# Kernel tuning notes

Measured on AMD Instinct MI355X. Metric: run time of the kernel, lower is better.

The kernel has to match this reference:

```python
import jax, jax.numpy as jnp
import numpy as np
from jax import lax

T, B, INP, HS, OUT = 256, 128, 1024, 1024, 1024


def setup_inputs() -> dict:
    key = jax.random.key(0)
    ks = jax.random.split(key, 7)
    s = 1.0 / np.sqrt(HS)  # scale params to keep tanh out of deep saturation
    return {
        "data": jax.random.normal(ks[0], (T, B, INP), jnp.float32),
        "W_ih": jax.random.normal(ks[1], (INP, HS), jnp.float32) * s,
        "W_hh": jax.random.normal(ks[2], (HS, HS), jnp.float32) * s,
        "b_i": jax.random.normal(ks[3], (HS,), jnp.float32) * s,
        "b_h": jax.random.normal(ks[4], (HS,), jnp.float32) * s,
        "W_out": jax.random.normal(ks[5], (OUT, HS), jnp.float32) * s,
        "b_out": jax.random.normal(ks[6], (OUT,), jnp.float32) * s,
    }


def reference(data, W_ih, W_hh, b_i, b_h, W_out, b_out):
    # Elman RNN: h_{t+1} = tanh(x_t @ W_ih + b_i + h_t @ W_hh + b_h)
    bias = b_i + b_h
    h0 = jnp.zeros((data.shape[1], W_hh.shape[0]), data.dtype)

    def step(h, x_t):
        h_new = jnp.tanh(x_t @ W_ih + h @ W_hh + bias)
        return h_new, None

    h_final, _ = lax.scan(step, h0, data)
    # nn.Linear: out = h @ W_out.T + b_out
    return h_final @ W_out.T + b_out
```

## Files before the change

### kernel.cpp

```cpp
#include <hip/hip_runtime.h>
#include <hip/hip_bf16.h>
#include <math.h>


typedef __attribute__((ext_vector_type(8))) short bf16x8;
typedef __attribute__((ext_vector_type(4))) float f32x4;
typedef __attribute__((ext_vector_type(4))) unsigned int u32x4;
typedef __attribute__((ext_vector_type(2))) unsigned int u32x2;

#define TT 256
#define BB 128
#define HS 1024
#define H_ELEMS (BB * HS)
#define POISON32 0xAAAAAAAAu

__device__ __forceinline__ short f2bf(float x) {
  __hip_bfloat16 b = __float2bfloat16(x);
  return *reinterpret_cast<short*>(&b);
}
__device__ __forceinline__ float bf2f(unsigned short s) {
  unsigned int u = ((unsigned int)s) << 16;
  float f;
  __builtin_memcpy(&f, &u, 4);
  return f;
}
__device__ __forceinline__ float fast_exp2(float x) {
#if __has_builtin(__builtin_amdgcn_exp2f)
  return __builtin_amdgcn_exp2f(x);
#else
  return exp2f(x);
#endif
}
__device__ __forceinline__ float fast_rcp(float x) {
#if __has_builtin(__builtin_amdgcn_rcpf)
  return __builtin_amdgcn_rcpf(x);
#else
  return 1.0f / x;
#endif
}
__device__ __forceinline__ float fast_tanh(float x) {
  float xc = fminf(fmaxf(x, -9.0f), 9.0f);
  float e = fast_exp2(2.8853900817779268f * xc);
  return (e - 1.0f) * fast_rcp(e + 1.0f);
}

__device__ __forceinline__ void mall_load_b128(u32x4* dst, const void* p) {
  asm volatile("global_load_dwordx4 %0, %1, off sc0 sc1" : "=v"(*dst) : "v"(p) : "memory");
}
__device__ __forceinline__ void mall_store_b64(void* p, u32x2 v) {
  asm volatile("global_store_dwordx2 %0, %1, off sc0 sc1" :: "v"(p), "v"(v) : "memory");
}
__device__ __forceinline__ void mall_store_b32(void* p, unsigned v) {
  asm volatile("global_store_dword %0, %1, off sc0 sc1" :: "v"(p), "v"(v) : "memory");
}
__device__ __forceinline__ unsigned mall_poll_b32(const void* p) {
  unsigned v;
  asm volatile("global_load_dword %0, %1, off sc0 sc1" : "=v"(v) : "v"(p) : "memory");
  asm volatile("s_waitcnt vmcnt(0)" : "+v"(v));
  return v;
}
__device__ __forceinline__ void wait_vm0() {
  asm volatile("s_waitcnt vmcnt(0)" ::: "memory");
}
#define TIE4(d)                                                         \
  asm volatile("s_waitcnt vmcnt(0)"                                     \
               : "+v"(d[0]), "+v"(d[1]), "+v"(d[2]), "+v"(d[3]))

__global__ __launch_bounds__(256) void cvt_data(const float* __restrict__ src,
                                                __hip_bfloat16* __restrict__ dst) {
  size_t i = ((size_t)blockIdx.x * 256 + threadIdx.x) * 8;
  f32x4 a = *reinterpret_cast<const f32x4*>(src + i);
  f32x4 b = *reinterpret_cast<const f32x4*>(src + i + 4);
  bf16x8 v;
  v[0] = f2bf(a[0]); v[1] = f2bf(a[1]); v[2] = f2bf(a[2]); v[3] = f2bf(a[3]);
  v[4] = f2bf(b[0]); v[5] = f2bf(b[1]); v[6] = f2bf(b[2]); v[7] = f2bf(b[3]);
  *reinterpret_cast<bf16x8*>(dst + i) = v;
}

__global__ __launch_bounds__(256) void cvt_tr(const float* __restrict__ src,
                                              __hip_bfloat16* __restrict__ dst) {
  __shared__ __hip_bfloat16 T[64][72];
  const int tid = threadIdx.x;
  const int k0 = blockIdx.y * 64, n0 = blockIdx.x * 64;
  const int r = tid >> 4, c4 = (tid & 15) * 4;
#pragma unroll
  for (int p = 0; p < 4; ++p) {
    int kk = r + p * 16;
    f32x4 v = *reinterpret_cast<const f32x4*>(src + (size_t)(k0 + kk) * 1024 + n0 + c4);
#pragma unroll
    for (int j = 0; j < 4; ++j) T[c4 + j][kk] = __float2bfloat16(v[j]);
  }
  __syncthreads();
  const int rr = tid >> 3, u = tid & 7;
#pragma unroll
  for (int p = 0; p < 2; ++p) {
    int R = rr + p * 32;
    *reinterpret_cast<bf16x8*>(dst + (size_t)(n0 + R) * 1024 + k0 + u * 8) =
        *reinterpret_cast<const bf16x8*>(&T[R][u * 8]);
  }
}

template <bool ABF>
__global__ __launch_bounds__(256) void gemm_xw2(
    const void* __restrict__ Ain,
    const __hip_bfloat16* __restrict__ Bt,
    const float* __restrict__ b_i,
    const float* __restrict__ b_h,
    __hip_bfloat16* __restrict__ P) {
  __shared__ __hip_bfloat16 As[128][72];
  __shared__ __hip_bfloat16 Bs[128][72];

  const int tid = threadIdx.x;
  const int m0 = blockIdx.y * 128, n0 = blockIdx.x * 128;
  const int wave = tid >> 6, lane = tid & 63;
  const int wm = wave & 1, wn = wave >> 1;
  const int quad = lane >> 4, l16 = lane & 15;
  const int sr = tid >> 3, su = tid & 7;

  f32x4 acc[4][4] = {};

  for (int k0 = 0; k0 < 1024; k0 += 64) {
    __syncthreads();
#pragma unroll
    for (int p = 0; p < 4; ++p) {
      int row = sr + p * 32;
      bf16x8 av;
      if (ABF) {
        av = *reinterpret_cast<const bf16x8*>(
            (const __hip_bfloat16*)Ain + (size_t)(m0 + row) * 1024 + k0 + su * 8);
      } else {
        const float* ap = (const float*)Ain + (size_t)(m0 + row) * 1024 + k0 + su * 8;
        f32x4 x = *reinterpret_cast<const f32x4*>(ap);
        f32x4 y = *reinterpret_cast<const f32x4*>(ap + 4);
        av[0] = f2bf(x[0]); av[1] = f2bf(x[1]); av[2] = f2bf(x[2]); av[3] = f2bf(x[3]);
        av[4] = f2bf(y[0]); av[5] = f2bf(y[1]); av[6] = f2bf(y[2]); av[7] = f2bf(y[3]);
      }
      *reinterpret_cast<bf16x8*>(&As[row][su * 8]) = av;
      bf16x8 bv = *reinterpret_cast<const bf16x8*>(
          Bt + (size_t)(n0 + row) * 1024 + k0 + su * 8);
      *reinterpret_cast<bf16x8*>(&Bs[row][su * 8]) = bv;
    }
    __syncthreads();
#pragma unroll
    for (int kk = 0; kk < 2; ++kk) {
      bf16x8 af[4], bfr[4];
#pragma unroll
      for (int mi = 0; mi < 4; ++mi)
        af[mi] = *reinterpret_cast<const bf16x8*>(&As[wm * 64 + mi * 16 + l16][kk * 32 + quad * 8]);
#pragma unroll
      for (int ni = 0; ni < 4; ++ni)
        bfr[ni] = *reinterpret_cast<const bf16x8*>(&Bs[wn * 64 + ni * 16 + l16][kk * 32 + quad * 8]);
#pragma unroll
      for (int mi = 0; mi < 4; ++mi)
#pragma unroll
        for (int ni = 0; ni < 4; ++ni)
          acc[mi][ni] = __builtin_amdgcn_mfma_f32_16x16x32_bf16(af[mi], bfr[ni], acc[mi][ni], 0, 0, 0);
    }
  }

  float bias[4];
#pragma unroll
  for (int ni = 0; ni < 4; ++ni) {
    int col = n0 + wn * 64 + ni * 16 + l16;
    bias[ni] = b_i[col] + b_h[col];
  }
#pragma unroll
  for (int mi = 0; mi < 4; ++mi)
#pragma unroll
    for (int ni = 0; ni < 4; ++ni) {
      int row = m0 + wm * 64 + mi * 16 + quad * 4;
      int col = n0 + wn * 64 + ni * 16 + l16;
#pragma unroll
      for (int r = 0; r < 4; ++r)
        P[(size_t)(row + r) * 1024 + col] = __float2bfloat16(acc[mi][ni][r] + bias[ni]);
    }
}

__global__ __launch_bounds__(512, 2) void rnn_scan8(
    const __hip_bfloat16* __restrict__ P,
    const float* __restrict__ W_hh,
    __hip_bfloat16* __restrict__ hslots) {
  __shared__ __hip_bfloat16 Wt[32 * 1024];
  __shared__ __hip_bfloat16 Ht[16 * 1024];
  __shared__ __hip_bfloat16 Cs[16 * 132];

  const int tid = threadIdx.x;
  const int m = blockIdx.x & 7;
  const int ng = blockIdx.x >> 3;
  const int m0 = m * 16, n0 = ng * 128;

  const int wv = tid >> 6, lane = tid & 63;
  const int quad = lane >> 4, l16 = lane & 15;
  const int colloc = wv * 16 + l16;
  const int col = n0 + colloc;
  const int nl = (wv & 1) * 16 + l16;
  const int xorl = l16 & 7;
  const int r16 = tid >> 5;
  const int s32 = tid & 31;

  bf16x8 wreg[32];
  for (int cch = 0; cch < 4; ++cch) {
    if (cch) __syncthreads();
    const int nb = n0 + cch * 32;
    for (int i = tid; i < 32 * 1024 / 4; i += 512) {
      int nq = i & 7, k = i >> 3;
      f32x4 v = *reinterpret_cast<const f32x4*>(W_hh + (size_t)k * 1024 + nb + nq * 4);
#pragma unroll
      for (int j = 0; j < 4; ++j) {
        int nll = nq * 4 + j;
        int sg = (k >> 3) ^ (nll & 7);
        Wt[nll * 1024 + sg * 8 + (k & 7)] = __float2bfloat16(v[j]);
      }
    }
    __syncthreads();
    if ((wv >> 1) == cch) {
#pragma unroll
      for (int wi = 0; wi < 32; ++wi) {
        int G = wi * 4 + quad;
        int sg = G ^ (nl & 7);
        wreg[wi] = *reinterpret_cast<const bf16x8*>(&Wt[nl * 1024 + sg * 8]);
      }
    }
  }
  __syncthreads();

  for (int t = 0; t < TT; ++t) {
    const __hip_bfloat16* hc = hslots + (size_t)t * H_ELEMS;
    __hip_bfloat16* hn = hslots + (size_t)(t + 1) * H_ELEMS;

    const __hip_bfloat16* Pt =
        P + (size_t)t * H_ELEMS + (size_t)(m0 + quad * 4) * 1024 + col;
    unsigned short pv[4];
#pragma unroll
    for (int r = 0; r < 4; ++r)
      pv[r] = *reinterpret_cast<const unsigned short*>(Pt + (size_t)r * 1024);

    const char* src = (const char*)(hc + (size_t)(m0 + r16) * 1024) + s32 * 16;
    u32x4 d[4];
    {
      int g = 0;
      for (;;) {
        mall_load_b128(&d[0], src);
        mall_load_b128(&d[1], src + 512);
        mall_load_b128(&d[2], src + 1024);
        mall_load_b128(&d[3], src + 1536);
        TIE4(d);
        bool ok = true;
#pragma unroll
        for (int i = 0; i < 4; ++i)
#pragma unroll
          for (int w2 = 0; w2 < 4; ++w2)
            ok &= (d[i][w2] != POISON32);
        if (ok || ++g >= (1 << 14)) break;
      }
    }
#pragma unroll
    for (int i = 0; i < 4; ++i) {
      int u = s32 + i * 32;
      int gp = u ^ (r16 & 7) ^ (u >> 4);
      *reinterpret_cast<u32x4*>(&Ht[r16 * 1024 + gp * 8]) = d[i];
    }
    __syncthreads();

    f32x4 acc[4] = {{0.f, 0.f, 0.f, 0.f}, {0.f, 0.f, 0.f, 0.f},
                    {0.f, 0.f, 0.f, 0.f}, {0.f, 0.f, 0.f, 0.f}};
#pragma unroll
    for (int c = 0; c < 8; ++c) {
#pragma unroll
      for (int j = 0; j < 4; ++j) {
        int G = c * 16 + j * 4 + quad;
        int gp = G ^ xorl ^ c;
        bf16x8 af = *reinterpret_cast<const bf16x8*>(&Ht[l16 * 1024 + gp * 8]);
        acc[j] = __builtin_amdgcn_mfma_f32_16x16x32_bf16(af, wreg[c * 4 + j], acc[j], 0, 0, 0);
      }
    }

#pragma unroll
    for (int r = 0; r < 4; ++r) {
      float s = (acc[0][r] + acc[1][r]) + (acc[2][r] + acc[3][r]) + bf2f(pv[r]);
      Cs[(quad * 4 + r) * 132 + colloc] = __float2bfloat16(fast_tanh(s));
    }
    __syncthreads();
    {
      u32x2 val = *reinterpret_cast<const u32x2*>(&Cs[r16 * 132 + s32 * 4]);
      mall_store_b64(hn + (size_t)(m0 + r16) * 1024 + n0 + s32 * 4, val);
    }
  }
  wait_vm0();
}

__global__ __launch_bounds__(512, 2) void rnn_scan7(
    const __hip_bfloat16* __restrict__ P,
    const float* __restrict__ W_hh,
    __hip_bfloat16* __restrict__ hbuf,
    unsigned* __restrict__ flags) {
  __shared__ __hip_bfloat16 Wt[32 * 1024];
  __shared__ __hip_bfloat16 Ht[16 * 1024];
  __shared__ __hip_bfloat16 Cs[16 * 132];

  const int tid = threadIdx.x;
  const int m = blockIdx.x & 7;
  const int ng = blockIdx.x >> 3;
  const int m0 = m * 16, n0 = ng * 128;

  const int wv = tid >> 6, lane = tid & 63;
  const int quad = lane >> 4, l16 = lane & 15;
  const int colloc = wv * 16 + l16;
  const int col = n0 + colloc;
  const int nl = (wv & 1) * 16 + l16;
  const int xorl = l16 & 7;
  const int r16 = tid >> 5;
  const int s32 = tid & 31;
  unsigned* gflags = flags + m * 8;

  bf16x8 wreg[32];
  for (int cch = 0; cch < 4; ++cch) {
    if (cch) __syncthreads();
    const int nb = n0 + cch * 32;
    for (int i = tid; i < 32 * 1024 / 4; i += 512) {
      int nq = i & 7, k = i >> 3;
      f32x4 v = *reinterpret_cast<const f32x4*>(W_hh + (size_t)k * 1024 + nb + nq * 4);
#pragma unroll
      for (int j = 0; j < 4; ++j) {
        int nll = nq * 4 + j;
        int sg = (k >> 3) ^ (nll & 7);
        Wt[nll * 1024 + sg * 8 + (k & 7)] = __float2bfloat16(v[j]);
      }
    }
    __syncthreads();
    if ((wv >> 1) == cch) {
#pragma unroll
      for (int wi = 0; wi < 32; ++wi) {
        int G = wi * 4 + quad;
        int sg = G ^ (nl & 7);
        wreg[wi] = *reinterpret_cast<const bf16x8*>(&Wt[nl * 1024 + sg * 8]);
      }
    }
  }
  __syncthreads();

  for (int t = 0; t < TT; ++t) {
    const __hip_bfloat16* hc = hbuf + (size_t)(t & 1) * H_ELEMS;
    __hip_bfloat16* hn = hbuf + (size_t)((t + 1) & 1) * H_ELEMS;

    const __hip_bfloat16* Pt =
        P + (size_t)t * H_ELEMS + (size_t)(m0 + quad * 4) * 1024 + col;
    unsigned short pv[4];
#pragma unroll
    for (int r = 0; r < 4; ++r)
      pv[r] = *reinterpret_cast<const unsigned short*>(Pt + (size_t)r * 1024);

    if (t > 0) {
      if (tid < 8) {
        const unsigned* fp = gflags + tid;
        int g = 0;
        while (mall_poll_b32(fp) < (unsigned)t && ++g < (1 << 18)) {}
      }
      __syncthreads();
    }

    {
      const char* src = (const char*)(hc + (size_t)(m0 + r16) * 1024) + s32 * 16;
      u32x4 d[4];
      mall_load_b128(&d[0], src);
      mall_load_b128(&d[1], src + 512);
      mall_load_b128(&d[2], src + 1024);
      mall_load_b128(&d[3], src + 1536);
      TIE4(d);
#pragma unroll
      for (int i = 0; i < 4; ++i) {
        int u = s32 + i * 32;
        int gp = u ^ (r16 & 7) ^ (u >> 4);
        *reinterpret_cast<u32x4*>(&Ht[r16 * 1024 + gp * 8]) = d[i];
      }
    }
    __syncthreads();

    f32x4 acc[4] = {{0.f, 0.f, 0.f, 0.f}, {0.f, 0.f, 0.f, 0.f},
                    {0.f, 0.f, 0.f, 0.f}, {0.f, 0.f, 0.f, 0.f}};
#pragma unroll
    for (int c = 0; c < 8; ++c) {
#pragma unroll
      for (int j = 0; j < 4; ++j) {
        int G = c * 16 + j * 4 + quad;
        int gp = G ^ xorl ^ c;
        bf16x8 af = *reinterpret_cast<const bf16x8*>(&Ht[l16 * 1024 + gp * 8]);
        acc[j] = __builtin_amdgcn_mfma_f32_16x16x32_bf16(af, wreg[c * 4 + j], acc[j], 0, 0, 0);
      }
    }

#pragma unroll
    for (int r = 0; r < 4; ++r) {
      float s = (acc[0][r] + acc[1][r]) + (acc[2][r] + acc[3][r]) + bf2f(pv[r]);
      Cs[(quad * 4 + r) * 132 + colloc] = __float2bfloat16(fast_tanh(s));
    }
    __syncthreads();
    {
      u32x2 val = *reinterpret_cast<const u32x2*>(&Cs[r16 * 132 + s32 * 4]);
      mall_store_b64(hn + (size_t)(m0 + r16) * 1024 + n0 + s32 * 4, val);
      wait_vm0();
    }
    __syncthreads();

    if (t != TT - 1 && tid == 0)
      mall_store_b32(gflags + ng, (unsigned)(t + 1));
  }
}

__global__ __launch_bounds__(256) void gemm_out(
    const __hip_bfloat16* __restrict__ h,
    const float* __restrict__ W_out,
    const float* __restrict__ b_out,
    float* __restrict__ out) {
  const int tid = threadIdx.x;
  const int wave = tid >> 6, lane = tid & 63;
  const int quad = lane >> 4, l16 = lane & 15;
  const int o = blockIdx.x * 64 + wave * 16 + l16;

  f32x4 acc[8] = {};
  for (int k0 = 0; k0 < 1024; k0 += 32) {
    f32x4 w0 = *reinterpret_cast<const f32x4*>(W_out + (size_t)o * 1024 + k0 + quad * 8);
    f32x4 w1 = *reinterpret_cast<const f32x4*>(W_out + (size_t)o * 1024 + k0 + quad * 8 + 4);
    bf16x8 bfr;
    bfr[0] = f2bf(w0[0]); bfr[1] = f2bf(w0[1]); bfr[2] = f2bf(w0[2]); bfr[3] = f2bf(w0[3]);
    bfr[4] = f2bf(w1[0]); bfr[5] = f2bf(w1[1]); bfr[6] = f2bf(w1[2]); bfr[7] = f2bf(w1[3]);
#pragma unroll
    for (int mi = 0; mi < 8; ++mi) {
      bf16x8 af = *reinterpret_cast<const bf16x8*>(h + (size_t)(mi * 16 + l16) * 1024 + k0 + quad * 8);
      acc[mi] = __builtin_amdgcn_mfma_f32_16x16x32_bf16(af, bfr, acc[mi], 0, 0, 0);
    }
  }
  const float bias = b_out[o];
#pragma unroll
  for (int mi = 0; mi < 8; ++mi)
#pragma unroll
    for (int r = 0; r < 4; ++r)
      out[(size_t)(mi * 16 + quad * 4 + r) * 1024 + o] = acc[mi][r] + bias;
}

extern "C" void kernel_launch(void* const* d_in, const int* in_sizes, int n_in,
                              void* d_out, int out_size, void* d_ws, size_t ws_size,
                              hipStream_t stream) {
  const float* data  = (const float*)d_in[0];
  const float* W_ih  = (const float*)d_in[1];
  const float* W_hh  = (const float*)d_in[2];
  const float* b_i   = (const float*)d_in[3];
  const float* b_h   = (const float*)d_in[4];
  const float* W_out = (const float*)d_in[5];
  const float* b_out = (const float*)d_in[6];
  float* out = (float*)d_out;

  char* ws = (char*)d_ws;
  const size_t OFF_P   = 0;
  const size_t OFF_H   = (size_t)TT * H_ELEMS * 2;
  const size_t OFF_FLG = OFF_H + 2 * H_ELEMS * 2;
  const size_t OFF_WT  = OFF_FLG + 1024;
  const size_t OFF_DB  = OFF_WT + 2u * 1024 * 1024;
  const size_t DB_B    = (size_t)TT * H_ELEMS * 2;

  const size_t SLOT_B  = (size_t)H_ELEMS * 2;
  const size_t SLOTS_B = (size_t)(TT + 1) * SLOT_B;
  const size_t OFF_S_SEP = OFF_DB + DB_B;
  const size_t NEED_SEP  = OFF_S_SEP + SLOTS_B;
  const size_t OFF_S_OVL = OFF_DB - SLOT_B;
  const size_t NEED_OVL  = OFF_DB + DB_B;

  __hip_bfloat16* P     = (__hip_bfloat16*)(ws + OFF_P);
  __hip_bfloat16* hbuf  = (__hip_bfloat16*)(ws + OFF_H);
  unsigned* flags       = (unsigned*)(ws + OFF_FLG);
  __hip_bfloat16* W_ihT = (__hip_bfloat16*)(ws + OFF_WT);
  __hip_bfloat16* dataB = (__hip_bfloat16*)(ws + OFF_DB);

  if (ws_size >= NEED_SEP) {
    __hip_bfloat16* slots = (__hip_bfloat16*)(ws + OFF_S_SEP);
    hipMemsetAsync(ws + OFF_S_SEP, 0, SLOT_B, stream);
    cvt_tr<<<dim3(16, 16), 256, 0, stream>>>(W_ih, W_ihT);
    cvt_data<<<16384, 256, 0, stream>>>(data, dataB);
    gemm_xw2<true><<<dim3(8, 256), 256, 0, stream>>>(dataB, W_ihT, b_i, b_h, P);
    rnn_scan8<<<64, 512, 0, stream>>>(P, W_hh, slots);
    gemm_out<<<16, 256, 0, stream>>>(slots + (size_t)TT * H_ELEMS, W_out, b_out, out);
  } else if (ws_size >= NEED_OVL) {
    __hip_bfloat16* slots = (__hip_bfloat16*)(ws + OFF_S_OVL);
    cvt_tr<<<dim3(16, 16), 256, 0, stream>>>(W_ih, W_ihT);
    cvt_data<<<16384, 256, 0, stream>>>(data, dataB);
    gemm_xw2<true><<<dim3(8, 256), 256, 0, stream>>>(dataB, W_ihT, b_i, b_h, P);
    hipMemsetAsync(ws + OFF_S_OVL, 0, SLOT_B, stream);
    hipMemsetAsync(ws + OFF_DB, 0xAA, DB_B, stream);
    rnn_scan8<<<64, 512, 0, stream>>>(P, W_hh, slots);
    gemm_out<<<16, 256, 0, stream>>>(slots + (size_t)TT * H_ELEMS, W_out, b_out, out);
  } else {
    hipMemsetAsync(ws + OFF_H, 0, 2 * H_ELEMS * 2 + 1024, stream);
    cvt_tr<<<dim3(16, 16), 256, 0, stream>>>(W_ih, W_ihT);
    gemm_xw2<false><<<dim3(8, 256), 256, 0, stream>>>(data, W_ihT, b_i, b_h, P);
    rnn_scan7<<<64, 512, 0, stream>>>(P, W_hh, hbuf, flags);
    gemm_out<<<16, 256, 0, stream>>>(hbuf, W_out, b_out, out);
  }
}
```

Measured before the change: 1.056 ms.

## Pre-transpose W_hh to bf16, prefetch next P, and use per-wave epilogue in scan

W_hh is converted and transposed to bf16 once in a separate kernel, so the scan kernel loads its weight registers straight from global memory instead of staging them through a 64KB LDS tile. With the smaller LDS footprint the launch bound drops to one block. The input projection for step t+1 is prefetched while step t runs. The output tile is staged per wave, so the post-tanh block barrier becomes a barrier before the epilogue. The cost is an extra transpose kernel and a reworked workspace layout, including which workspace is filled with the poison pattern.

```diff
diff --git a/kernel.cpp b/kernel.cpp
--- a/kernel.cpp
+++ b/kernel.cpp
@@ -176,13 +176,12 @@
     }
 }
 
-__global__ __launch_bounds__(512, 2) void rnn_scan8(
+__global__ __launch_bounds__(512, 1) void rnn_scan9(
     const __hip_bfloat16* __restrict__ P,
-    const float* __restrict__ W_hh,
+    const __hip_bfloat16* __restrict__ W_hhT,
     __hip_bfloat16* __restrict__ hslots) {
-  __shared__ __hip_bfloat16 Wt[32 * 1024];
   __shared__ __hip_bfloat16 Ht[16 * 1024];
-  __shared__ __hip_bfloat16 Cs[16 * 132];
+  __shared__ __hip_bfloat16 Csw[8][16][20];
 
   const int tid = threadIdx.x;
   const int m = blockIdx.x & 7;
@@ -193,47 +192,28 @@
   const int quad = lane >> 4, l16 = lane & 15;
   const int colloc = wv * 16 + l16;
   const int col = n0 + colloc;
-  const int nl = (wv & 1) * 16 + l16;
   const int xorl = l16 & 7;
   const int r16 = tid >> 5;
   const int s32 = tid & 31;
+  const int erow = lane >> 2, eseg = lane & 3;
 
   bf16x8 wreg[32];
-  for (int cch = 0; cch < 4; ++cch) {
-    if (cch) __syncthreads();
-    const int nb = n0 + cch * 32;
-    for (int i = tid; i < 32 * 1024 / 4; i += 512) {
-      int nq = i & 7, k = i >> 3;
-      f32x4 v = *reinterpret_cast<const f32x4*>(W_hh + (size_t)k * 1024 + nb + nq * 4);
-#pragma unroll
-      for (int j = 0; j < 4; ++j) {
-        int nll = nq * 4 + j;
-        int sg = (k >> 3) ^ (nll & 7);
-        Wt[nll * 1024 + sg * 8 + (k & 7)] = __float2bfloat16(v[j]);
-      }
-    }
-    __syncthreads();
-    if ((wv >> 1) == cch) {
-#pragma unroll
-      for (int wi = 0; wi < 32; ++wi) {
-        int G = wi * 4 + quad;
-        int sg = G ^ (nl & 7);
-        wreg[wi] = *reinterpret_cast<const bf16x8*>(&Wt[nl * 1024 + sg * 8]);
-      }
-    }
-  }
-  __syncthreads();
+#pragma unroll
+  for (int wi = 0; wi < 32; ++wi)
+    wreg[wi] = *reinterpret_cast<const bf16x8*>(
+        W_hhT + (size_t)col * 1024 + wi * 32 + quad * 8);
+
+  unsigned short pvA[4], pvB[4];
+  {
+    const __hip_bfloat16* Pt0 = P + (size_t)(m0 + quad * 4) * 1024 + col;
+#pragma unroll
+    for (int r = 0; r < 4; ++r)
+      pvA[r] = *reinterpret_cast<const unsigned short*>(Pt0 + (size_t)r * 1024);
+  }
 
   for (int t = 0; t < TT; ++t) {
     const __hip_bfloat16* hc = hslots + (size_t)t * H_ELEMS;
     __hip_bfloat16* hn = hslots + (size_t)(t + 1) * H_ELEMS;
-
-    const __hip_bfloat16* Pt =
-        P + (size_t)t * H_ELEMS + (size_t)(m0 + quad * 4) * 1024 + col;
-    unsigned short pv[4];
-#pragma unroll
-    for (int r = 0; r < 4; ++r)
-      pv[r] = *reinterpret_cast<const unsigned short*>(Pt + (size_t)r * 1024);
 
     const char* src = (const char*)(hc + (size_t)(m0 + r16) * 1024) + s32 * 16;
     u32x4 d[4];
@@ -254,6 +234,16 @@
         if (ok || ++g >= (1 << 14)) break;
       }
     }
+
+    {
+      int tn = (t + 1 < TT) ? t + 1 : TT - 1;
+      const __hip_bfloat16* Ptn =
+          P + (size_t)tn * H_ELEMS + (size_t)(m0 + quad * 4) * 1024 + col;
+#pragma unroll
+      for (int r = 0; r < 4; ++r)
+        pvB[r] = *reinterpret_cast<const unsigned short*>(Ptn + (size_t)r * 1024);
+    }
+
 #pragma unroll
     for (int i = 0; i < 4; ++i) {
       int u = s32 + i * 32;
@@ -274,17 +264,20 @@
         acc[j] = __builtin_amdgcn_mfma_f32_16x16x32_bf16(af, wreg[c * 4 + j], acc[j], 0, 0, 0);
       }
     }
+    __syncthreads();
 
 #pragma unroll
     for (int r = 0; r < 4; ++r) {
-      float s = (acc[0][r] + acc[1][r]) + (acc[2][r] + acc[3][r]) + bf2f(pv[r]);
-      Cs[(quad * 4 + r) * 132 + colloc] = __float2bfloat16(fast_tanh(s));
-    }
-    __syncthreads();
+      float s = (acc[0][r] + acc[1][r]) + (acc[2][r] + acc[3][r]) + bf2f(pvA[r]);
+      Csw[wv][quad * 4 + r][l16] = __float2bfloat16(fast_tanh(s));
+    }
     {
-      u32x2 val = *reinterpret_cast<const u32x2*>(&Cs[r16 * 132 + s32 * 4]);
-      mall_store_b64(hn + (size_t)(m0 + r16) * 1024 + n0 + s32 * 4, val);
-    }
+      u32x2 val = *reinterpret_cast<const u32x2*>(&Csw[wv][erow][eseg * 4]);
+      mall_store_b64(hn + (size_t)(m0 + erow) * 1024 + n0 + wv * 16 + eseg * 4, val);
+    }
+
+#pragma unroll
+    for (int r = 0; r < 4; ++r) pvA[r] = pvB[r];
   }
   wait_vm0();
 }
@@ -455,38 +448,41 @@
   const size_t OFF_H   = (size_t)TT * H_ELEMS * 2;
   const size_t OFF_FLG = OFF_H + 2 * H_ELEMS * 2;
   const size_t OFF_WT  = OFF_FLG + 1024;
-  const size_t OFF_DB  = OFF_WT + 2u * 1024 * 1024;
+  const size_t OFF_WH  = OFF_WT + 2u * 1024 * 1024;
+  const size_t OFF_DB  = OFF_WH + 2u * 1024 * 1024;
   const size_t DB_B    = (size_t)TT * H_ELEMS * 2;
 
   const size_t SLOT_B  = (size_t)H_ELEMS * 2;
   const size_t SLOTS_B = (size_t)(TT + 1) * SLOT_B;
   const size_t OFF_S_SEP = OFF_DB + DB_B;
   const size_t NEED_SEP  = OFF_S_SEP + SLOTS_B;
-  const size_t OFF_S_OVL = OFF_DB - SLOT_B;
-  const size_t NEED_OVL  = OFF_DB + DB_B;
+  const size_t NEED_OVL  = OFF_DB + SLOTS_B;
 
   __hip_bfloat16* P     = (__hip_bfloat16*)(ws + OFF_P);
   __hip_bfloat16* hbuf  = (__hip_bfloat16*)(ws + OFF_H);
   unsigned* flags       = (unsigned*)(ws + OFF_FLG);
   __hip_bfloat16* W_ihT = (__hip_bfloat16*)(ws + OFF_WT);
+  __hip_bfloat16* W_hhT = (__hip_bfloat16*)(ws + OFF_WH);
   __hip_bfloat16* dataB = (__hip_bfloat16*)(ws + OFF_DB);
 
   if (ws_size >= NEED_SEP) {
     __hip_bfloat16* slots = (__hip_bfloat16*)(ws + OFF_S_SEP);
     hipMemsetAsync(ws + OFF_S_SEP, 0, SLOT_B, stream);
     cvt_tr<<<dim3(16, 16), 256, 0, stream>>>(W_ih, W_ihT);
+    cvt_tr<<<dim3(16, 16), 256, 0, stream>>>(W_hh, W_hhT);
     cvt_data<<<16384, 256, 0, stream>>>(data, dataB);
     gemm_xw2<true><<<dim3(8, 256), 256, 0, stream>>>(dataB, W_ihT, b_i, b_h, P);
-    rnn_scan8<<<64, 512, 0, stream>>>(P, W_hh, slots);
+    rnn_scan9<<<64, 512, 0, stream>>>(P, W_hhT, slots);
     gemm_out<<<16, 256, 0, stream>>>(slots + (size_t)TT * H_ELEMS, W_out, b_out, out);
   } else if (ws_size >= NEED_OVL) {
-    __hip_bfloat16* slots = (__hip_bfloat16*)(ws + OFF_S_OVL);
+    __hip_bfloat16* slots = (__hip_bfloat16*)(ws + OFF_DB);
     cvt_tr<<<dim3(16, 16), 256, 0, stream>>>(W_ih, W_ihT);
+    cvt_tr<<<dim3(16, 16), 256, 0, stream>>>(W_hh, W_hhT);
     cvt_data<<<16384, 256, 0, stream>>>(data, dataB);
     gemm_xw2<true><<<dim3(8, 256), 256, 0, stream>>>(dataB, W_ihT, b_i, b_h, P);
-    hipMemsetAsync(ws + OFF_S_OVL, 0, SLOT_B, stream);
-    hipMemsetAsync(ws + OFF_DB, 0xAA, DB_B, stream);
-    rnn_scan8<<<64, 512, 0, stream>>>(P, W_hh, slots);
+    hipMemsetAsync(ws + OFF_DB, 0, SLOT_B, stream);
+    hipMemsetAsync(ws + OFF_DB + SLOT_B, 0xAA, SLOTS_B - SLOT_B, stream);
+    rnn_scan9<<<64, 512, 0, stream>>>(P, W_hhT, slots);
     gemm_out<<<16, 256, 0, stream>>>(slots + (size_t)TT * H_ELEMS, W_out, b_out, out);
   } else {
     hipMemsetAsync(ws + OFF_H, 0, 2 * H_ELEMS * 2 + 1024, stream);
```

New measurement: 972.2 us. 8.0% less time.
